# Kernel tuning notes

Measured on AMD Instinct MI355X. Metric: run time of the kernel, lower is better.

Reference implementation:

```python
import math
import jax, jax.numpy as jnp
import numpy as np

EMB = 768
N_HEAD = 12
B, T = 8, 1024

def setup_inputs() -> dict:
    key = jax.random.key(0)
    ks = jax.random.split(key, 5)
    x = jax.random.normal(ks[0], (B, T, EMB), dtype=jnp.float32)
    # linear params (torch nn.Linear: y = x @ W.T + b); store as [in, out] for einsum
    s1 = 1.0 / math.sqrt(EMB)
    W_attn = jax.random.uniform(ks[1], (EMB, 3 * EMB), jnp.float32, -s1, s1)
    b_attn = jax.random.uniform(ks[2], (3 * EMB,), jnp.float32, -s1, s1)
    W_proj = jax.random.uniform(ks[3], (EMB, EMB), jnp.float32, -s1, s1)
    b_proj = jax.random.uniform(ks[4], (EMB,), jnp.float32, -s1, s1)
    return {"x": x, "W_attn": W_attn, "b_attn": b_attn, "W_proj": W_proj, "b_proj": b_proj}

def reference(x, W_attn, b_attn, W_proj, b_proj):
    Bb, Tt, C = x.shape
    hd = C // N_HEAD
    qkv = x @ W_attn + b_attn                       # [B,T,3C]
    q, k, v = jnp.split(qkv, 3, axis=-1)
    # [B,T,C] -> [B,H,T,hd]
    def to_heads(t):
        return t.reshape(Bb, Tt, N_HEAD, hd).transpose(0, 2, 1, 3)
    q, k, v = to_heads(q), to_heads(k), to_heads(v)
    scale = 1.0 / math.sqrt(hd)
    scores = jnp.einsum('bhqd,bhkd->bhqk', q, k) * scale   # [B,H,T,T]
    causal = jnp.tril(jnp.ones((Tt, Tt), dtype=bool))
    scores = jnp.where(causal[None, None], scores, jnp.float32(-jnp.inf))
    attn = jax.nn.softmax(scores, axis=-1)
    y = jnp.einsum('bhqk,bhkd->bhqd', attn, v)              # [B,H,T,hd]
    y = y.transpose(0, 2, 1, 3).reshape(Bb, Tt, C)
    return y @ W_proj + b_proj
```

## Files before the change

kernel.cpp:

```cpp
#include <hip/hip_runtime.h>
#include <hip/hip_bf16.h>

typedef __hip_bfloat16 bf16;
typedef __attribute__((ext_vector_type(8))) short  bfrag;
typedef __attribute__((ext_vector_type(4))) float  facc;
typedef __attribute__((ext_vector_type(4))) short  short4v;

#define B_   8
#define T_   1024
#define C_   768
#define H_   12
#define HD_  64
#define M_   (B_ * T_)
#define N3_  (3 * C_)

#define QSCALE_ 0.18033688011112042f
#define M2_     17.312340490667562f

__device__ __forceinline__ float fexp2(float x) { return __builtin_amdgcn_exp2f(x); }

__device__ __forceinline__ void gload_lds16(const bf16* g, bf16* l) {
    __builtin_amdgcn_global_load_lds((const __attribute__((address_space(1))) void*)g,
                                     (__attribute__((address_space(3))) void*)l, 16, 0, 0);
}
__device__ __forceinline__ short bfbits(float f) {
    bf16 b = __float2bfloat16(f);
    return *reinterpret_cast<short*>(&b);
}

#define XBLK 6144
#define WABLK 1728
__global__ __launch_bounds__(256) void cvt_all_kernel(
        const float* __restrict__ x,  bf16* __restrict__ xb,
        const float* __restrict__ wa, bf16* __restrict__ wat,
        const float* __restrict__ wp, bf16* __restrict__ wpt) {
    const int bid = blockIdx.x, t = threadIdx.x;
    if (bid < XBLK) {
        const size_t i = ((size_t)bid * 256 + t) * 4;
        const float4 v = *(const float4*)(x + i);
        bf16* o = xb + i;
        o[0] = __float2bfloat16(v.x); o[1] = __float2bfloat16(v.y);
        o[2] = __float2bfloat16(v.z); o[3] = __float2bfloat16(v.w);
        return;
    }
    __shared__ float tile[32][33];
    const float* w; bf16* wt; int N, tI;
    if (bid < XBLK + WABLK) { w = wa; wt = wat; N = N3_; tI = bid - XBLK; }
    else                    { w = wp; wt = wpt; N = C_;  tI = bid - XBLK - WABLK; }
    const int ntn = N / 32;
    const int n0 = (tI % ntn) * 32, k0 = (tI / ntn) * 32;
    const int tx = t & 31, ty = t >> 5;
    for (int i = ty; i < 32; i += 8) tile[i][tx] = w[(size_t)(k0 + i) * N + n0 + tx];
    __syncthreads();
    for (int i = ty; i < 32; i += 8)
        wt[(size_t)(n0 + i) * C_ + k0 + tx] = __float2bfloat16(tile[tx][i]);
}


template<bool SWAPPED>
__device__ __forceinline__ void gemm96_core(
        const bf16* __restrict__ Ap, const bf16* __restrict__ Bp,
        const int m0, const int n0, const int kt0,
        bf16* smem, facc (&acc)[4][3]) {
    constexpr int KD = 768, NT = 12;
    bf16* As = smem;
    bf16* Bs = smem + 2 * 8192;
    const int t = threadIdx.x, w = t >> 6, lane = t & 63;
    const int wrow = (w >> 1) * 64;
    const int wcol = (w & 1) * 48;
    const int fr = lane & 15, quad = lane >> 4;
    const int pc0 = (quad ^ (fr & 7)) * 8;
    const int pc1 = ((quad + 4) ^ (fr & 7)) * 8;
    const int srow = t >> 3;
    const int schunk = ((t & 7) ^ (srow & 7)) * 8;
    const int sdo = t * 8;

    const bf16* Ag = Ap + (size_t)(m0 + srow) * KD + schunk;
    const bf16* Bg = Bp + (size_t)(n0 + srow) * KD + schunk;

#pragma unroll
    for (int i = 0; i < 4; ++i)
#pragma unroll
        for (int c = 0; c < 3; ++c)
#pragma unroll
            for (int r = 0; r < 4; ++r) acc[i][c][r] = 0.f;

    auto stageA = [&](bf16* dst, int k0) {
        const bf16* s = Ag + k0;
        bf16* d = dst + sdo;
#pragma unroll
        for (int r = 0; r < 4; ++r)
            gload_lds16(s + (size_t)(r * 32) * KD, d + r * 2048);
    };
    auto stageB = [&](bf16* dst, int k0) {
        const bf16* s = Bg + k0;
        bf16* d = dst + sdo;
#pragma unroll
        for (int r = 0; r < 3; ++r)
            gload_lds16(s + (size_t)(r * 32) * KD, d + r * 2048);
    };

    stageA(As, kt0 * 64);
    stageB(Bs, kt0 * 64);
    __syncthreads();

    int kt = kt0;
#pragma unroll 2
    for (int s = 0; s < NT; ++s) {
        const int cb = s & 1;
        const bf16* AsC = As + cb * 8192;
        const bf16* BsC = Bs + cb * 6144;
        const int ktn = (kt + 1 == NT) ? 0 : kt + 1;
        if (s + 1 < NT) {
            stageA(As + (cb ^ 1) * 8192, ktn * 64);
            stageB(Bs + (cb ^ 1) * 6144, ktn * 64);
        }
        bfrag af[4][2];
#pragma unroll
        for (int i = 0; i < 4; ++i) {
            const bf16* ar = AsC + (wrow + i * 16 + fr) * 64;
            af[i][0] = *(const bfrag*)(ar + pc0);
            af[i][1] = *(const bfrag*)(ar + pc1);
        }
#pragma unroll
        for (int c = 0; c < 3; ++c) {
            const bf16* br = BsC + (wcol + c * 16 + fr) * 64;
            bfrag b0 = *(const bfrag*)(br + pc0);
            bfrag b1 = *(const bfrag*)(br + pc1);
#pragma unroll
            for (int i = 0; i < 4; ++i) {
                if constexpr (SWAPPED) {
                    acc[i][c] = __builtin_amdgcn_mfma_f32_16x16x32_bf16(b0, af[i][0], acc[i][c], 0, 0, 0);
                    acc[i][c] = __builtin_amdgcn_mfma_f32_16x16x32_bf16(b1, af[i][1], acc[i][c], 0, 0, 0);
                } else {
                    acc[i][c] = __builtin_amdgcn_mfma_f32_16x16x32_bf16(af[i][0], b0, acc[i][c], 0, 0, 0);
                    acc[i][c] = __builtin_amdgcn_mfma_f32_16x16x32_bf16(af[i][1], b1, acc[i][c], 0, 0, 0);
                }
            }
        }
        __syncthreads();
        kt = ktn;
    }
}

__global__ __launch_bounds__(256, 2) void qkv_s_kernel(
        const bf16* __restrict__ xb, const bf16* __restrict__ wat,
        const float* __restrict__ bias,
        bf16* __restrict__ Q, bf16* __restrict__ K, bf16* __restrict__ Vt) {
    extern __shared__ bf16 smem[];
    const int id = blockIdx.x;
    const int wg = (id & 7) * 192 + (id >> 3);
    const int bx = wg % 24, by = wg / 24;
    const int m0 = by * 128, n0 = bx * 96;
    const int kt0 = (id >> 3) % 12;
    const int which = n0 / C_;

    facc acc[4][3];
    if (which < 2) gemm96_core<true >(xb, wat, m0, n0, kt0, smem, acc);
    else           gemm96_core<false>(xb, wat, m0, n0, kt0, smem, acc);

    const int t = threadIdx.x, w = t >> 6, lane = t & 63;
    const int wr = (w >> 1) * 64, wc = (w & 1) * 48;
    const int fr = lane & 15, quad = lane >> 4;
    const int bb = m0 >> 10;
    if (which < 2) {
        bf16* dst = which ? K : Q;
        const float sc = which ? 1.0f : QSCALE_;
#pragma unroll
        for (int i = 0; i < 4; ++i) {
            const int tt = (m0 & 1023) + wr + i * 16 + fr;
#pragma unroll
            for (int c = 0; c < 3; ++c) {
                const int colbase = n0 + wc + c * 16 + quad * 4;
                const int cc = colbase - which * C_;
                const int h = cc >> 6, d0 = cc & 63;
                const float4 bv = *(const float4*)(bias + colbase);
                short4v pk;
                pk[0] = bfbits((acc[i][c][0] + bv.x) * sc);
                pk[1] = bfbits((acc[i][c][1] + bv.y) * sc);
                pk[2] = bfbits((acc[i][c][2] + bv.z) * sc);
                pk[3] = bfbits((acc[i][c][3] + bv.w) * sc);
                *(short4v*)(dst + ((size_t)(bb * H_ + h) * T_ + tt) * HD_ + d0) = pk;
            }
        }
    } else {
#pragma unroll
        for (int i = 0; i < 4; ++i) {
            const int tt0 = (m0 & 1023) + wr + i * 16 + quad * 4;
#pragma unroll
            for (int c = 0; c < 3; ++c) {
                const int col = n0 + wc + c * 16 + fr;
                const int cc = col - 2 * C_;
                const int h = cc >> 6, d = cc & 63;
                const float bv = bias[col];
                short4v pk;
                pk[0] = bfbits(acc[i][c][0] + bv);
                pk[1] = bfbits(acc[i][c][1] + bv);
                pk[2] = bfbits(acc[i][c][2] + bv);
                pk[3] = bfbits(acc[i][c][3] + bv);
                *(short4v*)(Vt + ((size_t)(bb * H_ + h) * HD_ + d) * T_ + tt0) = pk;
            }
        }
    }
}

__global__ __launch_bounds__(256, 2) void proj_s_kernel(
        const bf16* __restrict__ y, const bf16* __restrict__ wpt,
        const float* __restrict__ bias, float* __restrict__ out) {
    extern __shared__ bf16 smem[];
    const int id = blockIdx.x;
    const int wg = (id & 7) * 64 + (id >> 3);
    const int bx = wg % 8, by = wg / 8;
    const int m0 = by * 128, n0 = bx * 96;
    const int kt0 = (id >> 3) % 12;

    facc acc[4][3];
    gemm96_core<true>(y, wpt, m0, n0, kt0, smem, acc);

    const int t = threadIdx.x, w = t >> 6, lane = t & 63;
    const int wr = (w >> 1) * 64, wc = (w & 1) * 48;
    const int fr = lane & 15, quad = lane >> 4;
#pragma unroll
    for (int i = 0; i < 4; ++i) {
        const int row = m0 + wr + i * 16 + fr;
#pragma unroll
        for (int c = 0; c < 3; ++c) {
            const int colbase = n0 + wc + c * 16 + quad * 4;
            const float4 bv = *(const float4*)(bias + colbase);
            float4 v;
            v.x = acc[i][c][0] + bv.x;
            v.y = acc[i][c][1] + bv.y;
            v.z = acc[i][c][2] + bv.z;
            v.w = acc[i][c][3] + bv.w;
            *(float4*)(out + (size_t)row * C_ + colbase) = v;
        }
    }
}

__global__ __launch_bounds__(256) void flash_attn_kernel(
        const bf16* __restrict__ Q, const bf16* __restrict__ K,
        const bf16* __restrict__ Vt, bf16* __restrict__ Y) {
    const int id   = blockIdx.x;
    const int bh   = (id & 7) * 12 + ((id >> 3) % 12);
    const int qpair = (id >> 3) / 12;
    const int t = threadIdx.x, w = t >> 6, lane = t & 63;
    const int fr = lane & 15, quad = lane >> 4, fq = quad * 8;

    __shared__ bf16 sK[2][64 * 64];
    __shared__ bf16 sVt[2][64 * 64];
    __shared__ bf16 sP[4][16][72];

    const bf16* Kbh = K  + (size_t)bh * T_ * HD_;
    const bf16* Vbh = Vt + (size_t)bh * HD_ * T_;
    const int b_ = bh / H_, h_ = bh % H_;

    const int srow = t >> 3;
    const int sgc  = ((t & 7) ^ (srow & 7)) * 8;
    const int c0   = (quad ^ (fr & 7)) * 8;

    for (int phase = 0; phase < 2; ++phase) {
        const int qt = (phase == 0) ? (15 - qpair) : qpair;
        const int q0 = qt * 64;

        const bf16* qbase = Q + ((size_t)bh * T_ + q0 + w * 16 + fr) * HD_;
        bfrag qa0 = *(const bfrag*)(qbase + fq);
        bfrag qa1 = *(const bfrag*)(qbase + 32 + fq);

        facc o[4];
        for (int nb = 0; nb < 4; ++nb) for (int r = 0; r < 4; ++r) o[nb][r] = 0.f;
        float rowl[4] = {0.f, 0.f, 0.f, 0.f};

        auto tile_step = [&](int kt, const bf16* sKp, const bf16* sVp) {
            const int k0 = kt * 64;
            facc s[4];
            for (int nb = 0; nb < 4; ++nb) for (int r = 0; r < 4; ++r) s[nb][r] = 0.f;
            __builtin_amdgcn_s_setprio(1);
            for (int nb = 0; nb < 4; ++nb) {
                const bf16* kr = sKp + (nb * 16 + fr) * 64;
                bfrag kb0 = *(const bfrag*)(kr + c0);
                bfrag kb1 = *(const bfrag*)(kr + (c0 ^ 32));
                s[nb] = __builtin_amdgcn_mfma_f32_16x16x32_bf16(qa0, kb0, s[nb], 0, 0, 0);
                s[nb] = __builtin_amdgcn_mfma_f32_16x16x32_bf16(qa1, kb1, s[nb], 0, 0, 0);
            }
            __builtin_amdgcn_s_setprio(0);
            const int mrow0 = q0 + w * 16 + quad * 4;
            float p[4][4];
            if (kt == qt) {
                for (int nb = 0; nb < 4; ++nb) {
                    const int n_g = k0 + nb * 16 + fr;
                    for (int r = 0; r < 4; ++r) {
                        const float a = (n_g > mrow0 + r) ? -1e30f : s[nb][r] - M2_;
                        p[nb][r] = fexp2(a);
                    }
                }
            } else {
                for (int nb = 0; nb < 4; ++nb)
                    for (int r = 0; r < 4; ++r)
                        p[nb][r] = fexp2(s[nb][r] - M2_);
            }
            for (int r = 0; r < 4; ++r)
                rowl[r] += p[0][r] + p[1][r] + p[2][r] + p[3][r];
            for (int nb = 0; nb < 4; ++nb)
                for (int r = 0; r < 4; ++r)
                    sP[w][quad * 4 + r][nb * 16 + fr] = __float2bfloat16(p[nb][r]);
            bfrag pa0 = *(const bfrag*)(&sP[w][fr][fq]);
            bfrag pa1 = *(const bfrag*)(&sP[w][fr][32 + fq]);
            __builtin_amdgcn_s_setprio(1);
            for (int nb = 0; nb < 4; ++nb) {
                const bf16* vr = sVp + (nb * 16 + fr) * 64;
                bfrag vb0 = *(const bfrag*)(vr + c0);
                bfrag vb1 = *(const bfrag*)(vr + (c0 ^ 32));
                o[nb] = __builtin_amdgcn_mfma_f32_16x16x32_bf16(pa0, vb0, o[nb], 0, 0, 0);
                o[nb] = __builtin_amdgcn_mfma_f32_16x16x32_bf16(pa1, vb1, o[nb], 0, 0, 0);
            }
            __builtin_amdgcn_s_setprio(0);
        };

        for (int kt = 0; kt <= qt; kt += 2) {
            const int k0 = kt * 64;
            const bool two = (kt + 1 <= qt);
            gload_lds16(Kbh + (size_t)(k0 + srow) * HD_ + sgc,      sK[0] + t * 8);
            gload_lds16(Kbh + (size_t)(k0 + 32 + srow) * HD_ + sgc, sK[0] + 2048 + t * 8);
            gload_lds16(Vbh + (size_t)srow * T_ + k0 + sgc,         sVt[0] + t * 8);
            gload_lds16(Vbh + (size_t)(srow + 32) * T_ + k0 + sgc,  sVt[0] + 2048 + t * 8);
            if (two) {
                const int k1 = k0 + 64;
                gload_lds16(Kbh + (size_t)(k1 + srow) * HD_ + sgc,      sK[1] + t * 8);
                gload_lds16(Kbh + (size_t)(k1 + 32 + srow) * HD_ + sgc, sK[1] + 2048 + t * 8);
                gload_lds16(Vbh + (size_t)srow * T_ + k1 + sgc,         sVt[1] + t * 8);
                gload_lds16(Vbh + (size_t)(srow + 32) * T_ + k1 + sgc,  sVt[1] + 2048 + t * 8);
            }
            __syncthreads();
            tile_step(kt, sK[0], sVt[0]);
            if (two) tile_step(kt + 1, sK[1], sVt[1]);
            __syncthreads();
        }

        for (int r = 0; r < 4; ++r) {
            float l = rowl[r];
            l += __shfl_xor(l, 1);
            l += __shfl_xor(l, 2);
            l += __shfl_xor(l, 4);
            l += __shfl_xor(l, 8);
            const float inv = 1.0f / l;
            const int tt = q0 + w * 16 + quad * 4 + r;
            bf16* yrow = Y + ((size_t)b_ * T_ + tt) * C_ + h_ * HD_;
            for (int nb = 0; nb < 4; ++nb)
                yrow[nb * 16 + fr] = __float2bfloat16(o[nb][r] * inv);
        }
    }
}

extern "C" void kernel_launch(void* const* d_in, const int* in_sizes, int n_in,
                              void* d_out, int out_size, void* d_ws, size_t ws_size,
                              hipStream_t stream) {
    const float* x      = (const float*)d_in[0];
    const float* W_attn = (const float*)d_in[1];
    const float* b_attn = (const float*)d_in[2];
    const float* W_proj = (const float*)d_in[3];
    const float* b_proj = (const float*)d_in[4];
    float* out = (float*)d_out;

    const size_t per = (size_t)B_ * H_ * T_ * HD_;
    bf16* Q   = (bf16*)d_ws;
    bf16* K   = Q + per;
    bf16* Vt  = K + per;
    bf16* XbY = Vt + per;
    bf16* WaT = XbY + per;
    bf16* WpT = WaT + (size_t)N3_ * C_;

    static bool s_attr = false;
    if (!s_attr) {
        hipFuncSetAttribute((const void*)qkv_s_kernel,
                            hipFuncAttributeMaxDynamicSharedMemorySize, 57344);
        hipFuncSetAttribute((const void*)proj_s_kernel,
                            hipFuncAttributeMaxDynamicSharedMemorySize, 57344);
        s_attr = true;
    }

    cvt_all_kernel<<<dim3(XBLK + WABLK + 576), dim3(256), 0, stream>>>(
        x, XbY, W_attn, WaT, W_proj, WpT);
    qkv_s_kernel<<<dim3(1536), dim3(256), 57344, stream>>>(
        XbY, WaT, b_attn, Q, K, Vt);
    flash_attn_kernel<<<dim3(768), dim3(256), 0, stream>>>(Q, K, Vt, XbY);
    proj_s_kernel<<<dim3(512), dim3(256), 57344, stream>>>(
        XbY, WpT, b_proj, out);
}
```

Before: 176.4 us.

## Widen QKV GEMM tile to 192 columns, use vmcnt waits and XCD-grouped block mapping

Generalizes the GEMM core over the N-tile width and doubles the QKV tile to 128x192, halving the grid to 768 blocks and raising LDS to 80KB. Replaces __syncthreads with explicit vmcnt waits plus raw s_barrier and setprio around the MFMA section, so the next tile's loads stay in flight. Remaps block IDs so each XCD covers a contiguous row/column group for L2 locality. The larger tile adds register and LDS pressure and may reduce occupancy.

```diff
diff --git a/kernel.cpp b/kernel.cpp
--- a/kernel.cpp
+++ b/kernel.cpp
@@ -57,17 +57,24 @@
 }
 
 
-template<bool SWAPPED>
-__device__ __forceinline__ void gemm96_core(
+#define WAIT_VM(N) asm volatile("s_waitcnt vmcnt(" #N ")" ::: "memory")
+
+template<int NB, bool SWAPPED>
+__device__ __forceinline__ void gemm_cv_core(
         const bf16* __restrict__ Ap, const bf16* __restrict__ Bp,
         const int m0, const int n0, const int kt0,
-        bf16* smem, facc (&acc)[4][3]) {
+        bf16* smem, facc (&acc)[4][NB / 2]) {
     constexpr int KD = 768, NT = 12;
+    constexpr int BN  = NB * 16;
+    constexpr int NC  = NB / 2;
+    constexpr int BSZ = BN * 64;
+    constexpr int LB  = BN / 32;
+    constexpr int LD  = 4 + LB;
     bf16* As = smem;
     bf16* Bs = smem + 2 * 8192;
     const int t = threadIdx.x, w = t >> 6, lane = t & 63;
     const int wrow = (w >> 1) * 64;
-    const int wcol = (w & 1) * 48;
+    const int wcol = (w & 1) * (NC * 16);
     const int fr = lane & 15, quad = lane >> 4;
     const int pc0 = (quad ^ (fr & 7)) * 8;
     const int pc1 = ((quad + 4) ^ (fr & 7)) * 8;
@@ -81,7 +88,7 @@
 #pragma unroll
     for (int i = 0; i < 4; ++i)
 #pragma unroll
-        for (int c = 0; c < 3; ++c)
+        for (int c = 0; c < NC; ++c)
 #pragma unroll
             for (int r = 0; r < 4; ++r) acc[i][c][r] = 0.f;
 
@@ -96,25 +103,30 @@
         const bf16* s = Bg + k0;
         bf16* d = dst + sdo;
 #pragma unroll
-        for (int r = 0; r < 3; ++r)
+        for (int r = 0; r < LB; ++r)
             gload_lds16(s + (size_t)(r * 32) * KD, d + r * 2048);
     };
 
     stageA(As, kt0 * 64);
     stageB(Bs, kt0 * 64);
-    __syncthreads();
 
     int kt = kt0;
 #pragma unroll 2
     for (int s = 0; s < NT; ++s) {
         const int cb = s & 1;
         const bf16* AsC = As + cb * 8192;
-        const bf16* BsC = Bs + cb * 6144;
+        const bf16* BsC = Bs + cb * BSZ;
         const int ktn = (kt + 1 == NT) ? 0 : kt + 1;
         if (s + 1 < NT) {
             stageA(As + (cb ^ 1) * 8192, ktn * 64);
-            stageB(Bs + (cb ^ 1) * 6144, ktn * 64);
-        }
+            stageB(Bs + (cb ^ 1) * BSZ,  ktn * 64);
+            if constexpr (LD == 10) WAIT_VM(10); else WAIT_VM(7);
+        } else {
+            WAIT_VM(0);
+        }
+        __builtin_amdgcn_s_barrier();
+        __builtin_amdgcn_sched_barrier(0);
+        __builtin_amdgcn_s_setprio(1);
         bfrag af[4][2];
 #pragma unroll
         for (int i = 0; i < 4; ++i) {
@@ -123,7 +135,7 @@
             af[i][1] = *(const bfrag*)(ar + pc1);
         }
 #pragma unroll
-        for (int c = 0; c < 3; ++c) {
+        for (int c = 0; c < NC; ++c) {
             const bf16* br = BsC + (wcol + c * 16 + fr) * 64;
             bfrag b0 = *(const bfrag*)(br + pc0);
             bfrag b1 = *(const bfrag*)(br + pc1);
@@ -138,29 +150,33 @@
                 }
             }
         }
-        __syncthreads();
+        __builtin_amdgcn_s_setprio(0);
+        __builtin_amdgcn_sched_barrier(0);
+        __builtin_amdgcn_s_barrier();
         kt = ktn;
     }
 }
 
-__global__ __launch_bounds__(256, 2) void qkv_s_kernel(
+__global__ __launch_bounds__(256, 2) void qkv_p_kernel(
         const bf16* __restrict__ xb, const bf16* __restrict__ wat,
         const float* __restrict__ bias,
         bf16* __restrict__ Q, bf16* __restrict__ K, bf16* __restrict__ Vt) {
     extern __shared__ bf16 smem[];
     const int id = blockIdx.x;
-    const int wg = (id & 7) * 192 + (id >> 3);
-    const int bx = wg % 24, by = wg / 24;
-    const int m0 = by * 128, n0 = bx * 96;
-    const int kt0 = (id >> 3) % 12;
-    const int which = n0 / C_;
-
-    facc acc[4][3];
-    if (which < 2) gemm96_core<true >(xb, wat, m0, n0, kt0, smem, acc);
-    else           gemm96_core<false>(xb, wat, m0, n0, kt0, smem, acc);
+    const int xcd = id & 7, L = id >> 3;
+    const int rgrp = xcd >> 1, cgrp = xcd & 1;
+    const int r_l = L & 15, c_l = L >> 4;
+    const int by = rgrp * 16 + r_l, bx = cgrp * 6 + c_l;
+    const int m0 = by * 128, n0 = bx * 192;
+    const int kt0 = L % 12;
+    const int which = bx / 4;
+
+    facc acc[4][6];
+    if (which < 2) gemm_cv_core<12, true >(xb, wat, m0, n0, kt0, smem, acc);
+    else           gemm_cv_core<12, false>(xb, wat, m0, n0, kt0, smem, acc);
 
     const int t = threadIdx.x, w = t >> 6, lane = t & 63;
-    const int wr = (w >> 1) * 64, wc = (w & 1) * 48;
+    const int wr = (w >> 1) * 64, wc = (w & 1) * 96;
     const int fr = lane & 15, quad = lane >> 4;
     const int bb = m0 >> 10;
     if (which < 2) {
@@ -170,7 +186,7 @@
         for (int i = 0; i < 4; ++i) {
             const int tt = (m0 & 1023) + wr + i * 16 + fr;
 #pragma unroll
-            for (int c = 0; c < 3; ++c) {
+            for (int c = 0; c < 6; ++c) {
                 const int colbase = n0 + wc + c * 16 + quad * 4;
                 const int cc = colbase - which * C_;
                 const int h = cc >> 6, d0 = cc & 63;
@@ -188,7 +204,7 @@
         for (int i = 0; i < 4; ++i) {
             const int tt0 = (m0 & 1023) + wr + i * 16 + quad * 4;
 #pragma unroll
-            for (int c = 0; c < 3; ++c) {
+            for (int c = 0; c < 6; ++c) {
                 const int col = n0 + wc + c * 16 + fr;
                 const int cc = col - 2 * C_;
                 const int h = cc >> 6, d = cc & 63;
@@ -204,18 +220,20 @@
     }
 }
 
-__global__ __launch_bounds__(256, 2) void proj_s_kernel(
+__global__ __launch_bounds__(256, 2) void proj_p_kernel(
         const bf16* __restrict__ y, const bf16* __restrict__ wpt,
         const float* __restrict__ bias, float* __restrict__ out) {
     extern __shared__ bf16 smem[];
     const int id = blockIdx.x;
-    const int wg = (id & 7) * 64 + (id >> 3);
-    const int bx = wg % 8, by = wg / 8;
+    const int xcd = id & 7, L = id >> 3;
+    const int rgrp = xcd >> 1, cgrp = xcd & 1;
+    const int r_l = L & 15, c_l = L >> 4;
+    const int by = rgrp * 16 + r_l, bx = cgrp * 4 + c_l;
     const int m0 = by * 128, n0 = bx * 96;
-    const int kt0 = (id >> 3) % 12;
+    const int kt0 = L % 12;
 
     facc acc[4][3];
-    gemm96_core<true>(y, wpt, m0, n0, kt0, smem, acc);
+    gemm_cv_core<6, true>(y, wpt, m0, n0, kt0, smem, acc);
 
     const int t = threadIdx.x, w = t >> 6, lane = t & 63;
     const int wr = (w >> 1) * 64, wc = (w & 1) * 48;
@@ -371,18 +389,18 @@
 
     static bool s_attr = false;
     if (!s_attr) {
-        hipFuncSetAttribute((const void*)qkv_s_kernel,
-                            hipFuncAttributeMaxDynamicSharedMemorySize, 57344);
-        hipFuncSetAttribute((const void*)proj_s_kernel,
+        hipFuncSetAttribute((const void*)qkv_p_kernel,
+                            hipFuncAttributeMaxDynamicSharedMemorySize, 81920);
+        hipFuncSetAttribute((const void*)proj_p_kernel,
                             hipFuncAttributeMaxDynamicSharedMemorySize, 57344);
         s_attr = true;
     }
 
     cvt_all_kernel<<<dim3(XBLK + WABLK + 576), dim3(256), 0, stream>>>(
         x, XbY, W_attn, WaT, W_proj, WpT);
-    qkv_s_kernel<<<dim3(1536), dim3(256), 57344, stream>>>(
+    qkv_p_kernel<<<dim3(768), dim3(256), 81920, stream>>>(
         XbY, WaT, b_attn, Q, K, Vt);
     flash_attn_kernel<<<dim3(768), dim3(256), 0, stream>>>(Q, K, Vt, XbY);
-    proj_s_kernel<<<dim3(512), dim3(256), 57344, stream>>>(
+    proj_p_kernel<<<dim3(512), dim3(256), 57344, stream>>>(
         XbY, WpT, b_proj, out);
 }
```

Result: faster. 171.4 us (-2.8%).
